# Optimization experiments

Hardware: AMD Instinct MI355X
Metric: run time of the kernel (lower is better)

## Reference

```python
import jax, jax.numpy as jnp
import numpy as np

TEMPERATURE = 1.0
BETA = 0.5
# D4 elements in the original enumeration order: [(k, flip) for flip in (False, True) for k in (0,1,2,3)]
ELEMENTS = [(k, f) for f in (False, True) for k in (0, 1, 2, 3)]


def _act(x, k, flip):
    y = jnp.flip(x, axis=-1) if flip else x
    k = k % 4
    if k:
        y = jnp.rot90(y, k, axes=(-2, -1))  # same convention as torch.rot90(dims=(-2,-1))
    return y


def setup_inputs() -> dict:
    key = jax.random.key(0)
    kx, kt = jax.random.split(key)
    x = jax.random.normal(kx, (16, 192, 224, 224), dtype=jnp.float32)
    theta = jax.random.normal(kt, (8,), dtype=jnp.float32)
    return {"x": x, "theta": theta}


def reference(x, theta):
    # weights over the 8 group elements
    w = jax.nn.softmax(theta / TEMPERATURE)
    y = jnp.zeros_like(x)
    for i, (k, f) in enumerate(ELEMENTS):  # fixed loop over 8 group elements
        y = y + w[i] * _act(x, k, f)
    # original divides by the detached running sum of used weights
    w_sum = jax.lax.stop_gradient(jnp.sum(w))
    y = y / jnp.maximum(w_sum, 1e-12)
    # residual mix
    return (1.0 - BETA) * x + BETA * y
```

## Files before the change

kernel.cpp:

```cpp
#include <hip/hip_runtime.h>
#include <hip/hip_bf16.h>

#define N 224
#define TS 32
#define NT 7
#define PITCH 33

constexpr int COMP[8][8] = {
    {0,1,2,3,4,5,6,7},
    {1,2,3,0,7,4,5,6},
    {2,3,0,1,6,7,4,5},
    {3,0,1,2,5,6,7,4},
    {4,5,6,7,0,1,2,3},
    {5,6,7,4,3,0,1,2},
    {6,7,4,5,2,3,0,1},
    {7,4,5,6,1,2,3,0},
};
constexpr int CAN[4][8] = {
    {0,1,2,3,4,5,6,7},
    {0,1,2,3,0,3,2,1},
    {0,1,2,3,1,0,3,2},
    {0,0,0,0,0,0,0,0},
};

template<int C, int NH, int NU>
__device__ __forceinline__ void orbit_compute(
        const float* __restrict__ plane, float* __restrict__ oplane,
        const float* c, float (*lds)[TS * PITCH],
        int I, int J, int row, int cg)
{
    const int rI = NT - 1 - I, rJ = NT - 1 - J;
    const int TI[8] = { I,  J, rI, rJ,  I,  J, rI, rJ };
    const int TJ[8] = { J, rI, rJ,  I, rJ,  I,  J, rI };

    #pragma unroll
    for (int u = 0; u < NU; ++u) {
        const float4 v = *reinterpret_cast<const float4*>(
            plane + (size_t)(TI[u] * TS + row) * N + TJ[u] * TS + cg);
        float* dst = &lds[u][row * PITCH + cg];
        dst[0] = v.x; dst[1] = v.y; dst[2] = v.z; dst[3] = v.w;
    }
    __syncthreads();

    const int ti = row, rti = TS - 1 - row;
    #pragma unroll
    for (int h = 0; h < NH; ++h) {
        float res[4];
        #pragma unroll
        for (int q = 0; q < 4; ++q) {
            const int tj = cg + q, rtj = TS - 1 - tj;
            res[q] =
                c[0] * lds[CAN[C][COMP[0][h]]][ti  * PITCH + tj ] +
                c[1] * lds[CAN[C][COMP[1][h]]][tj  * PITCH + rti] +
                c[2] * lds[CAN[C][COMP[2][h]]][rti * PITCH + rtj] +
                c[3] * lds[CAN[C][COMP[3][h]]][rtj * PITCH + ti ] +
                c[4] * lds[CAN[C][COMP[4][h]]][ti  * PITCH + rtj] +
                c[5] * lds[CAN[C][COMP[5][h]]][tj  * PITCH + ti ] +
                c[6] * lds[CAN[C][COMP[6][h]]][rti * PITCH + tj ] +
                c[7] * lds[CAN[C][COMP[7][h]]][rtj * PITCH + rti];
        }
        *reinterpret_cast<float4*>(
            oplane + (size_t)(TI[h] * TS + row) * N + TJ[h] * TS + cg)
            = make_float4(res[0], res[1], res[2], res[3]);
    }
}

__global__ __launch_bounds__(256, 4) void popmi_kernel(
        const float* __restrict__ x, const float* __restrict__ theta,
        float* __restrict__ out)
{
    __shared__ float lds[8][TS * PITCH];

    float th[8];
    #pragma unroll
    for (int i = 0; i < 8; ++i) th[i] = theta[i];
    float m = th[0];
    #pragma unroll
    for (int i = 1; i < 8; ++i) m = fmaxf(m, th[i]);
    float e[8], S = 0.f;
    #pragma unroll
    for (int i = 0; i < 8; ++i) { e[i] = expf(th[i] - m); S += e[i]; }
    float w[8], ws = 0.f;
    #pragma unroll
    for (int i = 0; i < 8; ++i) { w[i] = e[i] / S; ws += w[i]; }
    const float s = 0.5f / fmaxf(ws, 1e-12f);
    float c[8];
    #pragma unroll
    for (int i = 0; i < 8; ++i) c[i] = s * w[i];
    c[0] += 0.5f;

    const int bid = blockIdx.x;
    const int p   = bid / 10;
    const int o   = bid - p * 10;

    const int I = (0x1A211040u >> (3 * o)) & 7;
    const int J = (0x1A21B691u >> (3 * o)) & 7;

    const float* plane  = x   + (size_t)p * (N * N);
    float*       oplane = out + (size_t)p * (N * N);

    const int tid = threadIdx.x;
    const int row = tid >> 3;
    const int cg  = (tid & 7) << 2;

    if (o < 3)      orbit_compute<0,8,8>(plane, oplane, c, lds, I, J, row, cg);
    else if (o < 6) orbit_compute<1,4,4>(plane, oplane, c, lds, I, J, row, cg);
    else if (o < 9) orbit_compute<2,4,4>(plane, oplane, c, lds, I, J, row, cg);
    else            orbit_compute<3,1,1>(plane, oplane, c, lds, I, J, row, cg);
}

extern "C" void kernel_launch(void* const* d_in, const int* in_sizes, int n_in,
                              void* d_out, int out_size, void* d_ws, size_t ws_size,
                              hipStream_t stream) {
    const float* x     = (const float*)d_in[0];
    const float* theta = (const float*)d_in[1];
    float* out = (float*)d_out;

    const int planes = in_sizes[0] / (N * N);
    popmi_kernel<<<planes * 10, 256, 0, stream>>>(x, theta, out);
}
```

Measured before the change: 236.6 us.

## Halve LDS footprint by staging 8-tile orbits in two phases with register accumulators

The shared buffer shrinks from eight tiles to four. Full 8-tile orbits now run in two phases: the first four tiles are loaded to LDS, the second four are prefetched into registers, and partial sums for all eight outputs are kept in a 32-float accumulator across phases. The aim is to lower LDS use per block so more blocks fit per CU, and launch bounds are raised to 5 blocks per SM to match. The smaller-orbit classes are merged into one runtime-selected path. The cost is an extra sync and much higher register pressure, which could cause spills or limit occupancy anyway.

```diff
diff --git a/kernel.cpp b/kernel.cpp
--- a/kernel.cpp
+++ b/kernel.cpp
@@ -23,53 +23,46 @@
     {0,0,0,0,0,0,0,0},
 };
 
-template<int C, int NH, int NU>
-__device__ __forceinline__ void orbit_compute(
-        const float* __restrict__ plane, float* __restrict__ oplane,
-        const float* c, float (*lds)[TS * PITCH],
-        int I, int J, int row, int cg)
+__device__ __forceinline__ int gidx(int g, int ti, int tj, int rti, int rtj) {
+    switch (g) {
+        case 0: return ti  * PITCH + tj;
+        case 1: return tj  * PITCH + rti;
+        case 2: return rti * PITCH + rtj;
+        case 3: return rtj * PITCH + ti;
+        case 4: return ti  * PITCH + rtj;
+        case 5: return tj  * PITCH + ti;
+        default: break;
+    }
+    return (g == 6) ? (rti * PITCH + tj) : (rtj * PITCH + rti);
+}
+
+template<int P>
+__device__ __forceinline__ void gen_phase(float (&acc)[8][4], const float* c,
+        const float (*lds)[TS * PITCH], int row, int cg)
 {
-    const int rI = NT - 1 - I, rJ = NT - 1 - J;
-    const int TI[8] = { I,  J, rI, rJ,  I,  J, rI, rJ };
-    const int TJ[8] = { J, rI, rJ,  I, rJ,  I,  J, rI };
-
-    #pragma unroll
-    for (int u = 0; u < NU; ++u) {
-        const float4 v = *reinterpret_cast<const float4*>(
-            plane + (size_t)(TI[u] * TS + row) * N + TJ[u] * TS + cg);
-        float* dst = &lds[u][row * PITCH + cg];
-        dst[0] = v.x; dst[1] = v.y; dst[2] = v.z; dst[3] = v.w;
-    }
-    __syncthreads();
-
     const int ti = row, rti = TS - 1 - row;
     #pragma unroll
-    for (int h = 0; h < NH; ++h) {
-        float res[4];
+    for (int h = 0; h < 8; ++h) {
         #pragma unroll
         for (int q = 0; q < 4; ++q) {
             const int tj = cg + q, rtj = TS - 1 - tj;
-            res[q] =
-                c[0] * lds[CAN[C][COMP[0][h]]][ti  * PITCH + tj ] +
-                c[1] * lds[CAN[C][COMP[1][h]]][tj  * PITCH + rti] +
-                c[2] * lds[CAN[C][COMP[2][h]]][rti * PITCH + rtj] +
-                c[3] * lds[CAN[C][COMP[3][h]]][rtj * PITCH + ti ] +
-                c[4] * lds[CAN[C][COMP[4][h]]][ti  * PITCH + rtj] +
-                c[5] * lds[CAN[C][COMP[5][h]]][tj  * PITCH + ti ] +
-                c[6] * lds[CAN[C][COMP[6][h]]][rti * PITCH + tj ] +
-                c[7] * lds[CAN[C][COMP[7][h]]][rtj * PITCH + rti];
+            float s = acc[h][q];
+            #pragma unroll
+            for (int g = 0; g < 8; ++g) {
+                if ((COMP[g][h] >> 2) == P) {
+                    s += c[g] * lds[COMP[g][h] & 3][gidx(g, ti, tj, rti, rtj)];
+                }
+            }
+            acc[h][q] = s;
         }
-        *reinterpret_cast<float4*>(
-            oplane + (size_t)(TI[h] * TS + row) * N + TJ[h] * TS + cg)
-            = make_float4(res[0], res[1], res[2], res[3]);
     }
 }
 
-__global__ __launch_bounds__(256, 4) void popmi_kernel(
+__global__ __launch_bounds__(256, 5) void popmi_kernel(
         const float* __restrict__ x, const float* __restrict__ theta,
         float* __restrict__ out)
 {
-    __shared__ float lds[8][TS * PITCH];
+    __shared__ float lds[4][TS * PITCH];
 
     float th[8];
     #pragma unroll
@@ -83,10 +76,10 @@
     float w[8], ws = 0.f;
     #pragma unroll
     for (int i = 0; i < 8; ++i) { w[i] = e[i] / S; ws += w[i]; }
-    const float s = 0.5f / fmaxf(ws, 1e-12f);
+    const float s0 = 0.5f / fmaxf(ws, 1e-12f);
     float c[8];
     #pragma unroll
-    for (int i = 0; i < 8; ++i) c[i] = s * w[i];
+    for (int i = 0; i < 8; ++i) c[i] = s0 * w[i];
     c[0] += 0.5f;
 
     const int bid = blockIdx.x;
@@ -95,6 +88,10 @@
 
     const int I = (0x1A211040u >> (3 * o)) & 7;
     const int J = (0x1A21B691u >> (3 * o)) & 7;
+    const int rI = NT - 1 - I, rJ = NT - 1 - J;
+
+    const int TI[8] = { I,  J, rI, rJ,  I,  J, rI, rJ };
+    const int TJ[8] = { J, rI, rJ,  I, rJ,  I,  J, rI };
 
     const float* plane  = x   + (size_t)p * (N * N);
     float*       oplane = out + (size_t)p * (N * N);
@@ -102,11 +99,80 @@
     const int tid = threadIdx.x;
     const int row = tid >> 3;
     const int cg  = (tid & 7) << 2;
+    const int ti  = row, rti = TS - 1 - row;
 
-    if (o < 3)      orbit_compute<0,8,8>(plane, oplane, c, lds, I, J, row, cg);
-    else if (o < 6) orbit_compute<1,4,4>(plane, oplane, c, lds, I, J, row, cg);
-    else if (o < 9) orbit_compute<2,4,4>(plane, oplane, c, lds, I, J, row, cg);
-    else            orbit_compute<3,1,1>(plane, oplane, c, lds, I, J, row, cg);
+    if (o < 3) {
+        #pragma unroll
+        for (int u = 0; u < 4; ++u) {
+            const float4 v = *reinterpret_cast<const float4*>(
+                plane + (size_t)(TI[u] * TS + row) * N + TJ[u] * TS + cg);
+            float* dst = &lds[u][row * PITCH + cg];
+            dst[0] = v.x; dst[1] = v.y; dst[2] = v.z; dst[3] = v.w;
+        }
+        __syncthreads();
+
+        float4 vb[4];
+        #pragma unroll
+        for (int u = 0; u < 4; ++u) {
+            vb[u] = *reinterpret_cast<const float4*>(
+                plane + (size_t)(TI[u + 4] * TS + row) * N + TJ[u + 4] * TS + cg);
+        }
+
+        float acc[8][4] = {{0.f}};
+        gen_phase<0>(acc, c, lds, row, cg);
+        __syncthreads();
+
+        #pragma unroll
+        for (int u = 0; u < 4; ++u) {
+            float* dst = &lds[u][row * PITCH + cg];
+            dst[0] = vb[u].x; dst[1] = vb[u].y; dst[2] = vb[u].z; dst[3] = vb[u].w;
+        }
+        __syncthreads();
+
+        gen_phase<1>(acc, c, lds, row, cg);
+
+        #pragma unroll
+        for (int h = 0; h < 8; ++h) {
+            *reinterpret_cast<float4*>(
+                oplane + (size_t)(TI[h] * TS + row) * N + TJ[h] * TS + cg)
+                = make_float4(acc[h][0], acc[h][1], acc[h][2], acc[h][3]);
+        }
+    } else {
+        const int cls = (o < 6) ? 1 : (o < 9) ? 2 : 3;
+        const int nu  = (cls == 3) ? 1 : 4;
+        const int nh  = (cls == 3) ? 1 : 4;
+
+        for (int u = 0; u < nu; ++u) {
+            const float4 v = *reinterpret_cast<const float4*>(
+                plane + (size_t)(TI[u] * TS + row) * N + TJ[u] * TS + cg);
+            float* dst = &lds[u][row * PITCH + cg];
+            dst[0] = v.x; dst[1] = v.y; dst[2] = v.z; dst[3] = v.w;
+        }
+        __syncthreads();
+
+        #pragma unroll
+        for (int h = 0; h < 4; ++h) {
+            if (h < nh) {
+                float res[4];
+                #pragma unroll
+                for (int q = 0; q < 4; ++q) {
+                    const int tj = cg + q, rtj = TS - 1 - tj;
+                    float acc0 = 0.f;
+                    #pragma unroll
+                    for (int g = 0; g < 8; ++g) {
+                        const int slot1 = CAN[1][COMP[g][h]];
+                        const int slot2 = CAN[2][COMP[g][h]];
+                        const int slot  = (cls == 1) ? slot1 : (cls == 2) ? slot2 : 0;
+                        acc0 += c[g] * lds[slot][gidx(g, ti, tj, rti, rtj)];
+                    }
+                    res[q] = acc0;
+                }
+                *reinterpret_cast<float4*>(
+                    oplane + (size_t)(TI[h] * TS + row) * N + TJ[h] * TS + cg)
+                    = make_float4(res[0], res[1], res[2], res[3]);
+            }
+        }
+    }
 }
 
 extern "C" void kernel_launch(void* const* d_in, const int* in_sizes, int n_in,
```

After: 492.2 us. 2.08x slower.
